# Kernel tuning notes

Measured on AMD Instinct MI355X. Metric: run time of the kernel, lower is better.

## Reference

```python
import jax, jax.numpy as jnp
import numpy as np

B, H, W, C = 32, 56, 56, 512
HEADS, WS, SS = 16, 7, 3
N = WS * WS            # window area = 49
HD = C // HEADS        # head dim = 32
HID = 4 * C            # mlp hidden = 2048
nWh, nWw = H // WS, W // WS
nW = nWh * nWw


def _rel_pos_index():
    # static (N, N) int index into relative_position_bias_table
    coords = np.stack(np.meshgrid(np.arange(WS), np.arange(WS), indexing='ij'))  # (2, WS, WS)
    cf = coords.reshape(2, -1)                       # (2, N)
    rel = (cf[:, :, None] - cf[:, None, :]).transpose(1, 2, 0).copy()  # (N, N, 2)
    rel[:, :, 0] += WS - 1
    rel[:, :, 1] += WS - 1
    rel[:, :, 0] *= 2 * WS - 1
    return rel.sum(-1)  # (N, N)


def _attn_mask():
    # static shifted-window attention mask, (nW, N, N) with 0 / -100
    img = np.zeros((H, W))
    cnt = 0
    for h0, h1 in ((0, H - WS), (H - WS, H - SS), (H - SS, H)):
        for w0, w1 in ((0, W - WS), (W - WS, W - SS), (W - SS, W)):
            img[h0:h1, w0:w1] = cnt
            cnt += 1
    mw = img.reshape(nWh, WS, nWw, WS).transpose(0, 2, 1, 3).reshape(-1, N)  # (nW, N)
    diff = mw[:, None, :] - mw[:, :, None]
    return np.where(diff != 0, -100.0, 0.0).astype(np.float32)

_REL_IDX = _rel_pos_index()
_MASK = _attn_mask()


def _ln(x, g, b, eps=1e-5):
    mu = x.mean(-1, keepdims=True)
    var = ((x - mu) ** 2).mean(-1, keepdims=True)
    return (x - mu) * jax.lax.rsqrt(var + eps) * g + b


def setup_inputs() -> dict:
    key = jax.random.key(0)
    ks = jax.random.split(key, 8)
    s = lambda k, shape: jax.random.normal(k, shape, jnp.float32) * 0.02
    return {
        'x': jax.random.normal(ks[0], (B, H, W, C), jnp.float32),
        'norm1_g': jnp.ones((C,), jnp.float32), 'norm1_b': jnp.zeros((C,), jnp.float32),
        'qkv_w': s(ks[1], (3 * C, C)), 'qkv_b': jnp.zeros((3 * C,), jnp.float32),
        'rel_pos_table': s(ks[2], ((2 * WS - 1) ** 2, HEADS)),
        'proj_w': s(ks[3], (C, C)), 'proj_b': jnp.zeros((C,), jnp.float32),
        'norm2_g': jnp.ones((C,), jnp.float32), 'norm2_b': jnp.zeros((C,), jnp.float32),
        'fc1_w': s(ks[4], (HID, C)), 'fc1_b': jnp.zeros((HID,), jnp.float32),
        'fc2_w': s(ks[5], (C, HID)), 'fc2_b': jnp.zeros((C,), jnp.float32),
    }


def reference(x, norm1_g, norm1_b, qkv_w, qkv_b, rel_pos_table, proj_w, proj_b,
              norm2_g, norm2_b, fc1_w, fc1_b, fc2_w, fc2_b):
    shortcut = x
    y = _ln(x, norm1_g, norm1_b)
    # cyclic shift
    y = jnp.roll(y, (-SS, -SS), axis=(1, 2))
    # window partition -> (B*nW, N, C)
    yw = y.reshape(B, nWh, WS, nWw, WS, C).transpose(0, 1, 3, 2, 4, 5).reshape(B * nW, N, C)
    # qkv projection
    qkv = yw @ qkv_w.T + qkv_b
    qkv = qkv.reshape(B * nW, N, 3, HEADS, HD).transpose(2, 0, 3, 1, 4)
    q, k, v = qkv[0], qkv[1], qkv[2]              # each (B*nW, HEADS, N, HD)
    scale = HD ** -0.5
    attn = jnp.einsum('bhqd,bhkd->bhqk', q * scale, k)  # (B*nW, HEADS, N, N)
    # relative position bias gather
    bias = rel_pos_table[jnp.asarray(_REL_IDX.reshape(-1))].reshape(N, N, HEADS)
    attn = attn + bias.transpose(2, 0, 1)[None]
    # shifted-window mask
    attn = attn.reshape(B, nW, HEADS, N, N) + jnp.asarray(_MASK)[None, :, None]
    attn = jax.nn.softmax(attn.reshape(B * nW, HEADS, N, N), axis=-1)
    o = jnp.einsum('bhqk,bhkd->bhqd', attn, v)
    o = o.transpose(0, 2, 1, 3).reshape(B * nW, N, C)
    o = o @ proj_w.T + proj_b
    # window reverse + reverse shift
    o = o.reshape(B, nWh, nWw, WS, WS, C).transpose(0, 1, 3, 2, 4, 5).reshape(B, H, W, C)
    o = jnp.roll(o, (SS, SS), axis=(1, 2))
    x = shortcut + o
    # MLP
    h = _ln(x, norm2_g, norm2_b)
    h = jax.nn.gelu(h @ fc1_w.T + fc1_b, approximate=False)
    h = h @ fc2_w.T + fc2_b
    return x + h
```

## Files before the change

kernel.cpp:

```cpp
#include <hip/hip_runtime.h>

#define Bb   32
#define Hh   56
#define Ww_  56
#define Cc   512
#define HEADS 16
#define WS   7
#define SS   3
#define Nn   49
#define HD   32
#define HID  2048
#define NWIN 2048
#define NTOK 100352
#define NTOKP 100416

typedef __attribute__((ext_vector_type(4))) float f32x4;
typedef __attribute__((ext_vector_type(8))) short bf16x8;

#define AS1 __attribute__((address_space(1)))
#define AS3 __attribute__((address_space(3)))

__device__ __forceinline__ ushort f2bf(float x) {
  union { float f; unsigned u; } un; un.f = x;
  unsigned u = un.u;
  return (ushort)((u + 0x7fffu + ((u >> 16) & 1u)) >> 16);
}

__global__ void cvtw4_kern(const float* __restrict__ s0, ushort* __restrict__ d0, int n0,
                           const float* __restrict__ s1, ushort* __restrict__ d1, int n1,
                           const float* __restrict__ s2, ushort* __restrict__ d2, int n2,
                           const float* __restrict__ s3, ushort* __restrict__ d3, int n3) {
  int i = blockIdx.x * 256 + threadIdx.x;
  int stride = gridDim.x * 256;
  for (int k = i; k < n0; k += stride) d0[k] = f2bf(s0[k]);
  for (int k = i; k < n1; k += stride) d1[k] = f2bf(s1[k]);
  for (int k = i; k < n2; k += stride) d2[k] = f2bf(s2[k]);
  for (int k = i; k < n3; k += stride) d3[k] = f2bf(s3[k]);
}

__global__ void prep_bias_kern(const float* __restrict__ table, float* __restrict__ be2) {
  int idx = blockIdx.x * 256 + threadIdx.x;
  int h = idx >> 12, q = (idx >> 6) & 63, t = idx & 63;
  int l15 = t >> 2, n = t & 3;
  int key = n * 16 + l15;
  float v = 0.f;
  if (q < Nn && key < Nn) {
    int qi = q / 7, qj = q - qi * 7;
    int ki = key / 7, kj = key - ki * 7;
    v = table[((qi - ki + 6) * 13 + (qj - kj + 6)) * HEADS + h];
  }
  be2[idx] = v;
}

template<int MODE>
__global__ __launch_bounds__(256) void ln_kern(const float* __restrict__ x,
    const float* __restrict__ g, const float* __restrict__ bsh,
    ushort* __restrict__ out)
{
  int row  = blockIdx.x * 4 + (threadIdx.x >> 6);
  int lane = threadIdx.x & 63;
  const float* src;
  if (MODE == 0) {
    unsigned w = (unsigned)row / 49u, n = (unsigned)row - w * 49u;
    unsigned bb = w >> 6, wi = w & 63;
    unsigned wh = wi >> 3, ww = wi & 7;
    unsigned i = n / 7u, j = n - i * 7u;
    unsigned sr = wh * 7 + i + SS; if (sr >= Hh) sr -= Hh;
    unsigned sc = ww * 7 + j + SS; if (sc >= Ww_) sc -= Ww_;
    src = x + ((size_t)(bb * Hh + sr) * Ww_ + sc) * Cc;
  } else {
    src = x + (size_t)row * Cc;
  }
  int c = lane * 8;
  f32x4 v0 = *(const f32x4*)(src + c);
  f32x4 v1 = *(const f32x4*)(src + c + 4);
  float s = 0.f, s2 = 0.f;
  #pragma unroll
  for (int e = 0; e < 4; ++e) { s += v0[e]; s2 += v0[e]*v0[e]; s += v1[e]; s2 += v1[e]*v1[e]; }
  #pragma unroll
  for (int off = 32; off; off >>= 1) { s += __shfl_xor(s, off); s2 += __shfl_xor(s2, off); }
  float mu = s * (1.f / 512.f);
  float rstd = rsqrtf(s2 * (1.f / 512.f) - mu * mu + 1e-5f);
  bf16x8 r;
  #pragma unroll
  for (int e = 0; e < 8; ++e) {
    float xv = (e < 4) ? v0[e] : v1[e - 4];
    r[e] = (short)f2bf((xv - mu) * rstd * g[c + e] + bsh[c + e]);
  }
  *(bf16x8*)(out + (size_t)row * Cc + c) = r;
}

template<int EPI>
__global__ __launch_bounds__(256, 2) void gemm_kern(
    const ushort* __restrict__ A, const ushort* __restrict__ Bw,
    const float* __restrict__ bias, int M, int N, int K,
    void* __restrict__ outp, const float* __restrict__ resid,
    ushort* __restrict__ qb, ushort* __restrict__ kb, ushort* __restrict__ vb)
{
  __shared__ ushort As[128 * 64];
  __shared__ ushort Bs[128 * 64];
  const int tid = threadIdx.x;
  const int wave = tid >> 6, lane = tid & 63;
  const int l15 = lane & 15, lhi = lane >> 4;
  const int sw7 = l15 & 7;

  int gx = gridDim.x;
  int nwg = gx * gridDim.y;
  int orig = blockIdx.y * gx + blockIdx.x;
  int cpx = nwg >> 3;
  int wg = (orig & 7) * cpx + (orig >> 3);
  int bx = wg % gx, by = wg / gx;
  const int brow = by * 128, bcol = bx * 128;

  const int wr = (wave >> 1) * 64, wc = (wave & 1) * 64;

  const int srow = lane >> 3;
  const int schk = ((lane & 7) ^ srow) * 8;
  const ushort* aG = A  + (size_t)(brow + srow) * K + schk;
  const ushort* bG = Bw + (size_t)(bcol + srow) * K + schk;

  f32x4 acc[4][4];
  #pragma unroll
  for (int m = 0; m < 4; ++m)
    #pragma unroll
    for (int n = 0; n < 4; ++n)
      acc[m][n] = (f32x4){0.f, 0.f, 0.f, 0.f};

  for (int k0 = 0; k0 < K; k0 += 64) {
    if (k0) __syncthreads();
    #pragma unroll
    for (int s = 0; s < 4; ++s) {
      int rg = (s * 4 + wave) * 8;
      __builtin_amdgcn_global_load_lds(
        (const AS1 void*)(aG + (size_t)rg * K + k0),
        (AS3 void*)&As[rg * 64], 16, 0, 0);
      __builtin_amdgcn_global_load_lds(
        (const AS1 void*)(bG + (size_t)rg * K + k0),
        (AS3 void*)&Bs[rg * 64], 16, 0, 0);
    }
    __syncthreads();
    #pragma unroll
    for (int kk = 0; kk < 2; ++kk) {
      bf16x8 af[4], bfr[4];
      #pragma unroll
      for (int m = 0; m < 4; ++m) {
        af[m]  = *(const bf16x8*)&As[(wr + m * 16 + l15) * 64 + (((kk * 4 + lhi) ^ sw7)) * 8];
        bfr[m] = *(const bf16x8*)&Bs[(wc + m * 16 + l15) * 64 + (((kk * 4 + lhi) ^ sw7)) * 8];
      }
      #pragma unroll
      for (int m = 0; m < 4; ++m)
        #pragma unroll
        for (int n = 0; n < 4; ++n)
          acc[m][n] = __builtin_amdgcn_mfma_f32_16x16x32_bf16(af[m], bfr[n], acc[m][n], 0, 0, 0);
    }
  }

  float bv[4];
  #pragma unroll
  for (int n = 0; n < 4; ++n) bv[n] = bias[bcol + wc + n * 16 + l15];
  #pragma unroll
  for (int m = 0; m < 4; ++m) {
    int rbase = brow + wr + m * 16 + lhi * 4;
    #pragma unroll
    for (int n = 0; n < 4; ++n) {
      int cc = bcol + wc + n * 16 + l15;
      #pragma unroll
      for (int j = 0; j < 4; ++j) {
        unsigned r = (unsigned)(rbase + j);
        float v = acc[m][n][j] + bv[n];
        if (EPI == 0) {
          int part = cc >> 9, head = (cc >> 5) & 15, d = cc & 31;
          ushort bvs = f2bf(v);
          if (part == 0)      qb[((size_t)head * NTOKP + r) * 32 + d] = bvs;
          else if (part == 1) kb[((size_t)head * NTOKP + r) * 32 + d] = bvs;
          else {
            unsigned w = r / 49u, nn = r - w * 49u;
            vb[(((size_t)(w * HEADS + head)) * 32 + d) * 64 + nn] = bvs;
          }
        } else if (EPI == 1) {
          float u2 = v * (1.5957691216f + 0.0713548162f * v * v);
          float gl = __fdividef(v, 1.0f + __expf(-u2));
          ((ushort*)outp)[(size_t)r * N + cc] = f2bf(gl);
        } else if (EPI == 2) {
          unsigned w = r / 49u, nn = r - w * 49u;
          unsigned bb = w >> 6, wi = w & 63;
          unsigned wh = wi >> 3, ww = wi & 7;
          unsigned ii = nn / 7u, jj = nn - ii * 7u;
          unsigned dr = wh * 7 + ii + SS; if (dr >= Hh) dr -= Hh;
          unsigned dc = ww * 7 + jj + SS; if (dc >= Ww_) dc -= Ww_;
          size_t p = ((size_t)bb * Hh + dr) * Ww_ + dc;
          ((float*)outp)[p * Cc + cc] = resid[p * Cc + cc] + v;
        } else {
          float* o = (float*)outp;
          size_t idx = (size_t)r * Cc + cc;
          o[idx] = o[idx] + v;
        }
      }
    }
  }
}

__global__ __launch_bounds__(256) void attn_kern(
    const ushort* __restrict__ qb, const ushort* __restrict__ kb,
    const ushort* __restrict__ vb, const float* __restrict__ be2,
    ushort* __restrict__ o_win)
{
  __shared__ ushort P[4][4096];
  const int wv = threadIdx.x >> 6, lane = threadIdx.x & 63;
  const int l15 = lane & 15, lhi = lane >> 4;
  const int w = blockIdx.x;
  const int head = blockIdx.y * 4 + wv;
  const int wi = w & 63, whh = wi >> 3, www = wi & 7;
  ushort* Pl = P[wv];

  int krg[4];
  #pragma unroll
  for (int n = 0; n < 4; ++n) {
    int key = n * 16 + l15;
    int rg = -1;
    if (key < Nn) {
      int ki = key / 7, kj = key - ki * 7;
      int rr = whh * 7 + ki, cc = www * 7 + kj;
      rg = (rr < 49 ? 0 : (rr < 53 ? 1 : 2)) * 3 + (cc < 49 ? 0 : (cc < 53 ? 1 : 2));
    }
    krg[n] = rg;
  }
  int qrg[4][4];
  #pragma unroll
  for (int m = 0; m < 4; ++m)
    #pragma unroll
    for (int j = 0; j < 4; ++j) {
      int q = m * 16 + lhi * 4 + j;
      int rg = -2;
      if (q < Nn) {
        int qi = q / 7, qj = q - qi * 7;
        int rr = whh * 7 + qi, cc = www * 7 + qj;
        rg = (rr < 49 ? 0 : (rr < 53 ? 1 : 2)) * 3 + (cc < 49 ? 0 : (cc < 53 ? 1 : 2));
      }
      qrg[m][j] = rg;
    }

  const ushort* qp = qb + ((size_t)head * NTOKP + (size_t)w * 49) * 32;
  const ushort* kp = kb + ((size_t)head * NTOKP + (size_t)w * 49) * 32;
  const ushort* vp = vb + (size_t)(w * HEADS + head) * 2048;
  const float*  bep = be2 + head * 4096;

  bf16x8 qf[4], kf[4];
  #pragma unroll
  for (int m = 0; m < 4; ++m) {
    qf[m] = *(const bf16x8*)(qp + (m * 16 + l15) * 32 + lhi * 8);
    kf[m] = *(const bf16x8*)(kp + (m * 16 + l15) * 32 + lhi * 8);
  }
  f32x4 sa[4][4];
  #pragma unroll
  for (int m = 0; m < 4; ++m)
    #pragma unroll
    for (int n = 0; n < 4; ++n)
      sa[m][n] = __builtin_amdgcn_mfma_f32_16x16x32_bf16(qf[m], kf[n],
                   (f32x4){0.f, 0.f, 0.f, 0.f}, 0, 0, 0);

  #pragma unroll
  for (int m = 0; m < 4; ++m)
    #pragma unroll
    for (int j = 0; j < 4; ++j) {
      int q = m * 16 + lhi * 4 + j;
      int qr = qrg[m][j];
      f32x4 bev = *(const f32x4*)(bep + q * 64 + l15 * 4);
      float vv[4];
      float mx = -1e30f;
      #pragma unroll
      for (int n = 0; n < 4; ++n) {
        float v;
        if (qr >= 0 && krg[n] >= 0) {
          v = sa[m][n][j] * 0.17677669529663687f + bev[n];
          if (qr != krg[n]) v -= 100.0f;
        } else v = -1e30f;
        vv[n] = v;
        mx = fmaxf(mx, v);
      }
      #pragma unroll
      for (int off = 8; off; off >>= 1) mx = fmaxf(mx, __shfl_xor(mx, off));
      float sum = 0.f;
      #pragma unroll
      for (int n = 0; n < 4; ++n) { float p = __expf(vv[n] - mx); vv[n] = p; sum += p; }
      #pragma unroll
      for (int off = 8; off; off >>= 1) sum += __shfl_xor(sum, off);
      float is = 1.0f / sum;
      #pragma unroll
      for (int n = 0; n < 4; ++n) {
        int bo = (q * 128 + (n * 16 + l15) * 2) ^ ((q & 7) << 4);
        *(ushort*)((char*)Pl + bo) = f2bf(vv[n] * is);
      }
    }

  bf16x8 vf[2][2];
  #pragma unroll
  for (int nt = 0; nt < 2; ++nt)
    #pragma unroll
    for (int kt = 0; kt < 2; ++kt)
      vf[nt][kt] = *(const bf16x8*)(vp + (nt * 16 + l15) * 64 + kt * 32 + lhi * 8);
  f32x4 oa[4][2];
  #pragma unroll
  for (int m = 0; m < 4; ++m)
    #pragma unroll
    for (int nt = 0; nt < 2; ++nt)
      oa[m][nt] = (f32x4){0.f, 0.f, 0.f, 0.f};
  #pragma unroll
  for (int m = 0; m < 4; ++m) {
    int row = m * 16 + l15;
    #pragma unroll
    for (int kt = 0; kt < 2; ++kt) {
      int bo = (row * 128 + kt * 64 + lhi * 16) ^ ((row & 7) << 4);
      bf16x8 pa = *(const bf16x8*)((char*)Pl + bo);
      #pragma unroll
      for (int nt = 0; nt < 2; ++nt)
        oa[m][nt] = __builtin_amdgcn_mfma_f32_16x16x32_bf16(pa, vf[nt][kt], oa[m][nt], 0, 0, 0);
    }
  }
  #pragma unroll
  for (int m = 0; m < 4; ++m) {
    int q0 = m * 16 + lhi * 4;
    #pragma unroll
    for (int nt = 0; nt < 2; ++nt) {
      int d = nt * 16 + l15;
      #pragma unroll
      for (int j = 0; j < 4; ++j) {
        int q = q0 + j;
        if (q < Nn)
          o_win[((size_t)w * Nn + q) * Cc + head * HD + d] = f2bf(oa[m][nt][j]);
      }
    }
  }
}

extern "C" void kernel_launch(void* const* d_in, const int* in_sizes, int n_in,
                              void* d_out, int out_size, void* d_ws, size_t ws_size,
                              hipStream_t stream) {
  const float* x      = (const float*)d_in[0];
  const float* n1g    = (const float*)d_in[1];
  const float* n1b    = (const float*)d_in[2];
  const float* qkv_w  = (const float*)d_in[3];
  const float* qkv_b  = (const float*)d_in[4];
  const float* relt   = (const float*)d_in[5];
  const float* proj_w = (const float*)d_in[6];
  const float* proj_b = (const float*)d_in[7];
  const float* n2g    = (const float*)d_in[8];
  const float* n2b    = (const float*)d_in[9];
  const float* fc1_w  = (const float*)d_in[10];
  const float* fc1_b  = (const float*)d_in[11];
  const float* fc2_w  = (const float*)d_in[12];
  const float* fc2_b  = (const float*)d_in[13];

  char* ws = (char*)d_ws;
  ushort* wq = (ushort*)ws; ws += (size_t)1536 * 512 * 2;
  ushort* wp = (ushort*)ws; ws += (size_t)512 * 512 * 2;
  ushort* w1 = (ushort*)ws; ws += (size_t)2048 * 512 * 2;
  ushort* w2 = (ushort*)ws; ws += (size_t)512 * 2048 * 2;
  float*  be = (float*)ws;  ws += (size_t)16 * 64 * 64 * 4;
  ushort* buf1 = (ushort*)ws; ws += (size_t)NTOK * 2048 * 2;
  ushort* qbuf = (ushort*)ws; ws += (size_t)16 * NTOKP * 32 * 2;
  ushort* kbuf = (ushort*)ws; ws += (size_t)16 * NTOKP * 32 * 2;
  ushort* vbuf = (ushort*)ws; ws += (size_t)NWIN * 16 * 32 * 64 * 2;
  ushort* yw = buf1;
  ushort* o_win = buf1;
  ushort* h1 = buf1;
  ushort* l2buf = qbuf;
  float* xout = (float*)d_out;

  cvtw4_kern<<<2048, 256, 0, stream>>>(qkv_w, wq, 1536 * 512,
                                       proj_w, wp, 512 * 512,
                                       fc1_w, w1, 2048 * 512,
                                       fc2_w, w2, 512 * 2048);
  prep_bias_kern<<<65536 / 256, 256, 0, stream>>>(relt, be);

  ln_kern<0><<<NTOK / 4, 256, 0, stream>>>(x, n1g, n1b, yw);
  gemm_kern<0><<<dim3(12, 784), 256, 0, stream>>>(yw, wq, qkv_b, NTOK, 1536, 512,
                                                  nullptr, nullptr, qbuf, kbuf, vbuf);
  attn_kern<<<dim3(NWIN, 4), 256, 0, stream>>>(qbuf, kbuf, vbuf, be, o_win);
  gemm_kern<2><<<dim3(4, 784), 256, 0, stream>>>(o_win, wp, proj_b, NTOK, 512, 512,
                                                 xout, x, nullptr, nullptr, nullptr);
  ln_kern<1><<<NTOK / 4, 256, 0, stream>>>(xout, n2g, n2b, l2buf);
  gemm_kern<1><<<dim3(16, 784), 256, 0, stream>>>(l2buf, w1, fc1_b, NTOK, 2048, 512,
                                                  h1, nullptr, nullptr, nullptr, nullptr);
  gemm_kern<3><<<dim3(4, 784), 256, 0, stream>>>(h1, w2, fc2_b, NTOK, 512, 2048,
                                                 xout, xout, nullptr, nullptr, nullptr);
}
```

Measured before the change: 1.327 ms.

## Pre-swizzle weights into MFMA fragment layout and load B directly from global

Weight conversion now writes bf16 weights in a per-lane MFMA fragment order, so each wave can read its B operands straight from global memory into registers. The B tile no longer goes through LDS, which halves shared memory use per block and removes the B LDS reads. The cost is that the weight loads become direct global loads issued before the barrier, so GEMM latency now depends on L2/cache hits on the weights, and B data is no longer shared between the two waves that use the same columns.

```diff
diff --git a/kernel.cpp b/kernel.cpp
--- a/kernel.cpp
+++ b/kernel.cpp
@@ -26,16 +26,33 @@
   return (ushort)((u + 0x7fffu + ((u >> 16) & 1u)) >> 16);
 }
 
-__global__ void cvtw4_kern(const float* __restrict__ s0, ushort* __restrict__ d0, int n0,
-                           const float* __restrict__ s1, ushort* __restrict__ d1, int n1,
-                           const float* __restrict__ s2, ushort* __restrict__ d2, int n2,
-                           const float* __restrict__ s3, ushort* __restrict__ d3, int n3) {
-  int i = blockIdx.x * 256 + threadIdx.x;
+__device__ __forceinline__ void cvt_frag_seg(const float* __restrict__ s, ushort* __restrict__ d,
+                                             int N, int K, int tid0, int stride) {
+  int nch = (N * K) >> 3;
+  int kc = K >> 3;
+  int kkt = K >> 5;
+  for (int c = tid0; c < nch; c += stride) {
+    int row = c / kc, col8 = c - row * kc;
+    int n0 = row >> 4, l15 = row & 15;
+    int kk = col8 >> 2, lhi = col8 & 3;
+    int lane = (lhi << 4) | l15;
+    const float* sp = s + (size_t)c * 8;
+    ushort* dp = d + (((size_t)(n0 * kkt + kk) * 64 + lane) * 8);
+    #pragma unroll
+    for (int e = 0; e < 8; ++e) dp[e] = f2bf(sp[e]);
+  }
+}
+
+__global__ void cvtwf_kern(const float* __restrict__ s0, ushort* __restrict__ d0,
+                           const float* __restrict__ s1, ushort* __restrict__ d1,
+                           const float* __restrict__ s2, ushort* __restrict__ d2,
+                           const float* __restrict__ s3, ushort* __restrict__ d3) {
+  int tid0 = blockIdx.x * 256 + threadIdx.x;
   int stride = gridDim.x * 256;
-  for (int k = i; k < n0; k += stride) d0[k] = f2bf(s0[k]);
-  for (int k = i; k < n1; k += stride) d1[k] = f2bf(s1[k]);
-  for (int k = i; k < n2; k += stride) d2[k] = f2bf(s2[k]);
-  for (int k = i; k < n3; k += stride) d3[k] = f2bf(s3[k]);
+  cvt_frag_seg(s0, d0, 1536, 512, tid0, stride);
+  cvt_frag_seg(s1, d1, 512, 512, tid0, stride);
+  cvt_frag_seg(s2, d2, 2048, 512, tid0, stride);
+  cvt_frag_seg(s3, d3, 512, 2048, tid0, stride);
 }
 
 __global__ void prep_bias_kern(const float* __restrict__ table, float* __restrict__ be2) {
@@ -92,13 +109,12 @@
 
 template<int EPI>
 __global__ __launch_bounds__(256, 2) void gemm_kern(
-    const ushort* __restrict__ A, const ushort* __restrict__ Bw,
+    const ushort* __restrict__ A, const ushort* __restrict__ Bf,
     const float* __restrict__ bias, int M, int N, int K,
     void* __restrict__ outp, const float* __restrict__ resid,
     ushort* __restrict__ qb, ushort* __restrict__ kb, ushort* __restrict__ vb)
 {
   __shared__ ushort As[128 * 64];
-  __shared__ ushort Bs[128 * 64];
   const int tid = threadIdx.x;
   const int wave = tid >> 6, lane = tid & 63;
   const int l15 = lane & 15, lhi = lane >> 4;
@@ -116,8 +132,11 @@
 
   const int srow = lane >> 3;
   const int schk = ((lane & 7) ^ srow) * 8;
-  const ushort* aG = A  + (size_t)(brow + srow) * K + schk;
-  const ushort* bG = Bw + (size_t)(bcol + srow) * K + schk;
+  const ushort* aG = A + (size_t)(brow + srow) * K + schk;
+
+  const int kkt = K >> 5;
+  const int nb0 = (bcol + wc) >> 4;
+  const ushort* bW = Bf + (size_t)nb0 * kkt * 512 + (size_t)lane * 8;
 
   f32x4 acc[4][4];
   #pragma unroll
@@ -134,24 +153,26 @@
       __builtin_amdgcn_global_load_lds(
         (const AS1 void*)(aG + (size_t)rg * K + k0),
         (AS3 void*)&As[rg * 64], 16, 0, 0);
-      __builtin_amdgcn_global_load_lds(
-        (const AS1 void*)(bG + (size_t)rg * K + k0),
-        (AS3 void*)&Bs[rg * 64], 16, 0, 0);
-    }
+    }
+    bf16x8 bfr[2][4];
+    const int kk0 = k0 >> 5;
+    #pragma unroll
+    for (int kk = 0; kk < 2; ++kk)
+      #pragma unroll
+      for (int n = 0; n < 4; ++n)
+        bfr[kk][n] = *(const bf16x8*)(bW + ((size_t)n * kkt + kk0 + kk) * 512);
     __syncthreads();
     #pragma unroll
     for (int kk = 0; kk < 2; ++kk) {
-      bf16x8 af[4], bfr[4];
-      #pragma unroll
-      for (int m = 0; m < 4; ++m) {
-        af[m]  = *(const bf16x8*)&As[(wr + m * 16 + l15) * 64 + (((kk * 4 + lhi) ^ sw7)) * 8];
-        bfr[m] = *(const bf16x8*)&Bs[(wc + m * 16 + l15) * 64 + (((kk * 4 + lhi) ^ sw7)) * 8];
-      }
+      bf16x8 af[4];
+      #pragma unroll
+      for (int m = 0; m < 4; ++m)
+        af[m] = *(const bf16x8*)&As[(wr + m * 16 + l15) * 64 + (((kk * 4 + lhi) ^ sw7)) * 8];
       #pragma unroll
       for (int m = 0; m < 4; ++m)
         #pragma unroll
         for (int n = 0; n < 4; ++n)
-          acc[m][n] = __builtin_amdgcn_mfma_f32_16x16x32_bf16(af[m], bfr[n], acc[m][n], 0, 0, 0);
+          acc[m][n] = __builtin_amdgcn_mfma_f32_16x16x32_bf16(af[m], bfr[kk][n], acc[m][n], 0, 0, 0);
     }
   }
 
@@ -367,10 +388,7 @@
   ushort* l2buf = qbuf;
   float* xout = (float*)d_out;
 
-  cvtw4_kern<<<2048, 256, 0, stream>>>(qkv_w, wq, 1536 * 512,
-                                       proj_w, wp, 512 * 512,
-                                       fc1_w, w1, 2048 * 512,
-                                       fc2_w, w2, 512 * 2048);
+  cvtwf_kern<<<2048, 256, 0, stream>>>(qkv_w, wq, proj_w, wp, fc1_w, w1, fc2_w, w2);
   prep_bias_kern<<<65536 / 256, 256, 0, stream>>>(relt, be);
 
   ln_kern<0><<<NTOK / 4, 256, 0, stream>>>(x, n1g, n1b, yw);
```

Result: no change. 1.327 ms (+0.0%).
